# Kernel optimization log

Hardware: AMD Instinct MI355X
Metric: run time of the kernel (lower is better)

## Reference

```python
import jax, jax.numpy as jnp
import numpy as np

N_NODES = 50000
N_EDGES = 800000
IN_CH = 128
HID = 16
HEADS = 8
OUT_CH = 64


def setup_inputs() -> dict:
    key = jax.random.key(0)
    ks = jax.random.split(key, 16)
    H1 = HID * HEADS  # 128
    inp = {
        "x": jax.random.normal(ks[0], (N_NODES, IN_CH), dtype=jnp.float32),
        "edge_index": jax.random.randint(ks[1], (2, N_EDGES), 0, N_NODES, dtype=jnp.int64),
        # layer 1: GATv2Conv(IN_CH -> HID, heads=HEADS, concat=True)
        "W1l": jax.random.normal(ks[2], (IN_CH, H1), dtype=jnp.float32) * 0.05,
        "W1r": jax.random.normal(ks[3], (IN_CH, H1), dtype=jnp.float32) * 0.05,
        "att1": jax.random.normal(ks[4], (HEADS, HID), dtype=jnp.float32) * 0.05,
        "b1": jnp.zeros((H1,), dtype=jnp.float32),
        "skip1_W": jax.random.normal(ks[5], (IN_CH, H1), dtype=jnp.float32) * 0.05,
        "skip1_b": jnp.zeros((H1,), dtype=jnp.float32),
        # PyG LayerNorm (default mode='graph') affine params
        "ln_w": jnp.ones((H1,), dtype=jnp.float32),
        "ln_b": jnp.zeros((H1,), dtype=jnp.float32),
        # layer 2: GATv2Conv(H1 -> OUT_CH, heads=1, concat=False)
        "W2l": jax.random.normal(ks[6], (H1, OUT_CH), dtype=jnp.float32) * 0.05,
        "W2r": jax.random.normal(ks[7], (H1, OUT_CH), dtype=jnp.float32) * 0.05,
        "att2": jax.random.normal(ks[8], (1, OUT_CH), dtype=jnp.float32) * 0.05,
        "b2": jnp.zeros((OUT_CH,), dtype=jnp.float32),
        "skip2_W": jax.random.normal(ks[9], (H1, OUT_CH), dtype=jnp.float32) * 0.05,
        "skip2_b": jnp.zeros((OUT_CH,), dtype=jnp.float32),
    }
    return inp


def _gatv2(x, src, dst, Wl, Wr, att, b, concat):
    # GATv2Conv message passing (PyG semantics, share_weights=False).
    N = x.shape[0]
    H, C = att.shape
    xl = (x @ Wl).reshape(N, H, C)  # source transform (lin_l)
    xr = (x @ Wr).reshape(N, H, C)  # target transform (lin_r)
    e = jax.nn.leaky_relu(xl[src] + xr[dst], 0.2)  # [E,H,C]
    a = jnp.einsum('ehc,hc->eh', e, att)  # attention logits [E,H]
    # segment softmax over incoming edges of each dst node (self-loops guarantee non-empty)
    m = jax.lax.stop_gradient(jax.ops.segment_max(a, dst, num_segments=N))
    p = jnp.exp(a - m[dst])
    denom = jax.ops.segment_sum(p, dst, num_segments=N)
    alpha = p / denom[dst]  # [E,H]
    out = jax.ops.segment_sum(alpha[:, :, None] * xl[src], dst, num_segments=N)  # [N,H,C]
    out = out.reshape(N, H * C) if concat else out.mean(axis=1)
    return out + b


def reference(x, edge_index, W1l, W1r, att1, b1, skip1_W, skip1_b,
              ln_w, ln_b, W2l, W2r, att2, b2, skip2_W, skip2_b):
    N = x.shape[0]
    loop = jnp.arange(N, dtype=edge_index.dtype)
    src = jnp.concatenate([edge_index[0], loop])  # add_self_loops=True (PyG default)
    dst = jnp.concatenate([edge_index[1], loop])

    # layer 1: conv + skip
    h = _gatv2(x, src, dst, W1l, W1r, att1, b1, True) + (x @ skip1_W + skip1_b)
    # PyG LayerNorm, mode='graph': normalize over all nodes and features of the graph
    mu = h.mean()
    var = jnp.mean((h - mu) ** 2)
    h = ln_w * (h - mu) / jnp.sqrt(var + 1e-5) + ln_b
    h = jax.nn.elu(h)
    # dropout: inference mode -> identity

    # layer 2: conv (heads=1, concat=False) + skip
    out = _gatv2(h, src, dst, W2l, W2r, att2, b2, False) + (h @ skip2_W + skip2_b)
    return out
```

## Files before the change

### kernel.cpp

```cpp
#include <hip/hip_runtime.h>
#include <math.h>

#define NND 50000
#define NE0 800000
#define NET 850000
#define SCAN_B 196

using short8 = __attribute__((ext_vector_type(8))) short;
using f32x4  = __attribute__((ext_vector_type(4))) float;

__device__ __forceinline__ float lrelu(float v) { return v > 0.f ? v : 0.2f * v; }

__device__ __forceinline__ unsigned short f2bf(float f) {
    unsigned int u = __float_as_uint(f);
    u = (u + 0x7fff + ((u >> 16) & 1)) >> 16;
    return (unsigned short)u;
}
__device__ __forceinline__ float2 bf2x2(unsigned int u) {
    float2 r;
    r.x = __uint_as_float(u << 16);
    r.y = __uint_as_float(u & 0xffff0000u);
    return r;
}

template <int CTRL>
__device__ __forceinline__ float dpp_add(float v) {
    int j = __builtin_amdgcn_update_dpp(0, __float_as_int(v), CTRL, 0xf, 0xf, true);
    return v + __int_as_float(j);
}

__global__ __launch_bounds__(256) void wt_prep(const float* __restrict__ S0,
                                               const float* __restrict__ S1,
                                               const float* __restrict__ S2,
                                               unsigned short* __restrict__ T0,
                                               unsigned short* __restrict__ T1,
                                               unsigned short* __restrict__ T2, int N) {
    int per = 128 * N, total = 3 * per;
    for (int idx = blockIdx.x * blockDim.x + threadIdx.x; idx < total;
         idx += gridDim.x * blockDim.x) {
        int which = idx / per;
        int rem = idx - which * per;
        int k = rem / N, n = rem - k * N;
        const float* S = which == 0 ? S0 : (which == 1 ? S1 : S2);
        unsigned short* T = which == 0 ? T0 : (which == 1 ? T1 : T2);
        T[n * 128 + k] = f2bf(S[rem]);
    }
}

template <int BN, bool LN>
__global__ __launch_bounds__(256) void gemm3_mfma(
    const float* __restrict__ A,
    const unsigned short* __restrict__ Bt0, const unsigned short* __restrict__ Bt1,
    const unsigned short* __restrict__ Bt2, const float* __restrict__ bias2,
    unsigned short* __restrict__ C0, unsigned short* __restrict__ C1, float* __restrict__ C2,
    const float* __restrict__ musig, const float* __restrict__ lnw,
    const float* __restrict__ lnb, int M) {
    __shared__ __align__(16) unsigned short As[64 * 128];
    const int tid = threadIdx.x;
    const int m0 = blockIdx.x * 64;

    float mu = 0.f, rinv = 1.f;
    if constexpr (LN) { mu = musig[0]; rinv = musig[1]; }

    {
        const int row = tid >> 2, qc = tid & 3;
        const int gm = m0 + row;
        const float* Ar = A + (size_t)gm * 128;
#pragma unroll
        for (int i = 0; i < 4; i++) {
            int k0 = qc * 32 + i * 8;
            float v[8];
            if (gm < M) {
                float4 a0 = *(const float4*)(Ar + k0);
                float4 a1 = *(const float4*)(Ar + k0 + 4);
                v[0] = a0.x; v[1] = a0.y; v[2] = a0.z; v[3] = a0.w;
                v[4] = a1.x; v[5] = a1.y; v[6] = a1.z; v[7] = a1.w;
            } else {
#pragma unroll
                for (int j = 0; j < 8; j++) v[j] = 0.f;
            }
            if constexpr (LN) {
                float4 w0 = *(const float4*)(lnw + k0);
                float4 w1 = *(const float4*)(lnw + k0 + 4);
                float4 b0 = *(const float4*)(lnb + k0);
                float4 b1 = *(const float4*)(lnb + k0 + 4);
                float wv[8] = {w0.x, w0.y, w0.z, w0.w, w1.x, w1.y, w1.z, w1.w};
                float bv[8] = {b0.x, b0.y, b0.z, b0.w, b1.x, b1.y, b1.z, b1.w};
#pragma unroll
                for (int j = 0; j < 8; j++) {
                    float t = wv[j] * (v[j] - mu) * rinv + bv[j];
                    v[j] = t > 0.f ? t : __expf(t) - 1.f;
                }
            }
            short8 pk;
#pragma unroll
            for (int j = 0; j < 8; j++) pk[j] = (short)f2bf(v[j]);
            *(short8*)&As[row * 128 + (k0 ^ ((row & 7) << 3))] = pk;
        }
    }
    __syncthreads();

    const int lane = tid & 63;
    const int wid = tid >> 6;
    const int lr = lane & 15;
    const int lk = lane >> 4;

    short8 a[4][4];
#pragma unroll
    for (int rf = 0; rf < 4; rf++) {
        int row = rf * 16 + lr;
#pragma unroll
        for (int kc = 0; kc < 4; kc++) {
            int k0 = kc * 32 + lk * 8;
            a[rf][kc] = *(short8*)&As[row * 128 + (k0 ^ ((row & 7) << 3))];
        }
    }

    constexpr int NCF = BN / 64;
    const int nbase = wid * (BN / 4);

    const unsigned short* Bts[3] = {Bt0, Bt1, Bt2};
#pragma unroll
    for (int j = 0; j < 3; j++) {
        const unsigned short* Bt = Bts[j];
        short8 b[NCF][4];
#pragma unroll
        for (int cf = 0; cf < NCF; cf++) {
            int n = nbase + cf * 16 + lr;
#pragma unroll
            for (int kc = 0; kc < 4; kc++)
                b[cf][kc] = *(const short8*)(Bt + (size_t)n * 128 + kc * 32 + lk * 8);
        }
        f32x4 acc[4][NCF];
#pragma unroll
        for (int rf = 0; rf < 4; rf++)
#pragma unroll
            for (int cf = 0; cf < NCF; cf++) acc[rf][cf] = (f32x4){0.f, 0.f, 0.f, 0.f};
#pragma unroll
        for (int kc = 0; kc < 4; kc++)
#pragma unroll
            for (int rf = 0; rf < 4; rf++)
#pragma unroll
                for (int cf = 0; cf < NCF; cf++)
                    acc[rf][cf] = __builtin_amdgcn_mfma_f32_16x16x32_bf16(
                        a[rf][kc], b[cf][kc], acc[rf][cf], 0, 0, 0);
        if (j < 2) {
            unsigned short* C = (j == 0) ? C0 : C1;
#pragma unroll
            for (int rf = 0; rf < 4; rf++)
#pragma unroll
                for (int cf = 0; cf < NCF; cf++) {
                    int col = nbase + cf * 16 + lr;
#pragma unroll
                    for (int r = 0; r < 4; r++) {
                        int row = m0 + rf * 16 + lk * 4 + r;
                        if (row < M) C[(size_t)row * BN + col] = f2bf(acc[rf][cf][r]);
                    }
                }
        } else {
#pragma unroll
            for (int rf = 0; rf < 4; rf++)
#pragma unroll
                for (int cf = 0; cf < NCF; cf++) {
                    int col = nbase + cf * 16 + lr;
                    float bb = bias2[col];
#pragma unroll
                    for (int r = 0; r < 4; r++) {
                        int row = m0 + rf * 16 + lk * 4 + r;
                        if (row < M) C2[(size_t)row * BN + col] = acc[rf][cf][r] + bb;
                    }
                }
        }
    }
}

__global__ __launch_bounds__(256) void csr_count(const int* __restrict__ ei, int* __restrict__ deg) {
    int i = blockIdx.x * blockDim.x + threadIdx.x;
    int stride = gridDim.x * blockDim.x;
    for (int e = i; e < NE0; e += stride) atomicAdd(&deg[ei[NE0 + e]], 1);
}

__global__ __launch_bounds__(256) void scan1(const int* __restrict__ deg,
                                             int* __restrict__ locexc,
                                             int* __restrict__ blocksum) {
    __shared__ int s[256];
    const int t = threadIdx.x;
    const int g = blockIdx.x * 256 + t;
    int v = (g < NND) ? deg[g] + 1 : 0;
    s[t] = v;
    __syncthreads();
    for (int off = 1; off < 256; off <<= 1) {
        int x = (t >= off) ? s[t - off] : 0;
        __syncthreads();
        s[t] += x;
        __syncthreads();
    }
    if (g < NND) locexc[g] = s[t] - v;
    if (t == 255) blocksum[blockIdx.x] = s[255];
}

__global__ __launch_bounds__(256) void scan2(const int* __restrict__ blocksum,
                                             int* __restrict__ blockoff,
                                             int* __restrict__ rowptr) {
    __shared__ int s[256];
    const int t = threadIdx.x;
    int v = (t < SCAN_B) ? blocksum[t] : 0;
    s[t] = v;
    __syncthreads();
    for (int off = 1; off < 256; off <<= 1) {
        int x = (t >= off) ? s[t - off] : 0;
        __syncthreads();
        s[t] += x;
        __syncthreads();
    }
    if (t < SCAN_B) blockoff[t] = s[t] - v;
    if (t == 255) rowptr[NND] = s[255];
}

__global__ __launch_bounds__(256) void scan3(const int* __restrict__ locexc,
                                             const int* __restrict__ blockoff,
                                             int* __restrict__ rowptr,
                                             int* __restrict__ csrs) {
    const int g = blockIdx.x * 256 + threadIdx.x;
    if (g < NND) {
        int rp = locexc[g] + blockoff[g >> 8];
        rowptr[g] = rp;
        csrs[rp] = g;
    }
}

__global__ __launch_bounds__(256) void csr_fill(const int* __restrict__ ei,
                                                const int* __restrict__ rowptr,
                                                int* __restrict__ cursor,
                                                int* __restrict__ csrs) {
    int i = blockIdx.x * blockDim.x + threadIdx.x;
    int stride = gridDim.x * blockDim.x;
    for (int e = i; e < NE0; e += stride) {
        int s = ei[e], d = ei[NE0 + e];
        int pos = atomicAdd(&cursor[d], 1);
        csrs[rowptr[d] + 1 + pos] = s;
    }
}

__global__ __launch_bounds__(256) void aggr_l1(const int* __restrict__ rowptr,
                                               const int* __restrict__ csrs,
                                               const unsigned short* __restrict__ xl,
                                               const unsigned short* __restrict__ xr,
                                               const float* __restrict__ att,
                                               const float* __restrict__ b1,
                                               float* __restrict__ h,
                                               float2* __restrict__ partial) {
    const int lane = threadIdx.x & 63;
    const int wv = threadIdx.x >> 6;
    int wid = (blockIdx.x * blockDim.x + threadIdx.x) >> 6;
    const int nw = (gridDim.x * blockDim.x) >> 6;
    const int c = lane * 2;
    float2 attv = *(const float2*)(att + c);
    float2 b1v = *(const float2*)(b1 + c);
    float ts = 0.f, ts2 = 0.f;
    for (int d = wid; d < NND; d += nw) {
        int p0 = rowptr[d], p1 = rowptr[d + 1];
        float2 xrv = bf2x2(*(const unsigned int*)(xr + (size_t)d * 128 + c));
        float den0 = 0.f, den1 = 0.f, den2 = 0.f, den3 = 0.f;
        float a00 = 0.f, a01 = 0.f, a10 = 0.f, a11 = 0.f;
        float a20 = 0.f, a21 = 0.f, a30 = 0.f, a31 = 0.f;
        int i = p0;
        for (; i + 4 <= p1; i += 4) {
            int s0 = csrs[i], s1 = csrs[i + 1], s2 = csrs[i + 2], s3 = csrs[i + 3];
            float2 x0 = bf2x2(*(const unsigned int*)(xl + (size_t)s0 * 128 + c));
            float2 x1 = bf2x2(*(const unsigned int*)(xl + (size_t)s1 * 128 + c));
            float2 x2 = bf2x2(*(const unsigned int*)(xl + (size_t)s2 * 128 + c));
            float2 x3 = bf2x2(*(const unsigned int*)(xl + (size_t)s3 * 128 + c));
            float q0 = lrelu(x0.x + xrv.x) * attv.x + lrelu(x0.y + xrv.y) * attv.y;
            float q1 = lrelu(x1.x + xrv.x) * attv.x + lrelu(x1.y + xrv.y) * attv.y;
            float q2 = lrelu(x2.x + xrv.x) * attv.x + lrelu(x2.y + xrv.y) * attv.y;
            float q3 = lrelu(x3.x + xrv.x) * attv.x + lrelu(x3.y + xrv.y) * attv.y;
            q0 = dpp_add<0xB1>(q0); q0 = dpp_add<0x4E>(q0); q0 = dpp_add<0x141>(q0);
            q1 = dpp_add<0xB1>(q1); q1 = dpp_add<0x4E>(q1); q1 = dpp_add<0x141>(q1);
            q2 = dpp_add<0xB1>(q2); q2 = dpp_add<0x4E>(q2); q2 = dpp_add<0x141>(q2);
            q3 = dpp_add<0xB1>(q3); q3 = dpp_add<0x4E>(q3); q3 = dpp_add<0x141>(q3);
            float p0v = __expf(q0), p1v = __expf(q1), p2v = __expf(q2), p3v = __expf(q3);
            den0 += p0v; a00 = fmaf(p0v, x0.x, a00); a01 = fmaf(p0v, x0.y, a01);
            den1 += p1v; a10 = fmaf(p1v, x1.x, a10); a11 = fmaf(p1v, x1.y, a11);
            den2 += p2v; a20 = fmaf(p2v, x2.x, a20); a21 = fmaf(p2v, x2.y, a21);
            den3 += p3v; a30 = fmaf(p3v, x3.x, a30); a31 = fmaf(p3v, x3.y, a31);
        }
        for (; i < p1; i++) {
            int s0 = csrs[i];
            float2 x0 = bf2x2(*(const unsigned int*)(xl + (size_t)s0 * 128 + c));
            float q0 = lrelu(x0.x + xrv.x) * attv.x + lrelu(x0.y + xrv.y) * attv.y;
            q0 = dpp_add<0xB1>(q0); q0 = dpp_add<0x4E>(q0); q0 = dpp_add<0x141>(q0);
            float p0v = __expf(q0);
            den0 += p0v; a00 = fmaf(p0v, x0.x, a00); a01 = fmaf(p0v, x0.y, a01);
        }
        float den = (den0 + den1) + (den2 + den3);
        float a0 = (a00 + a10) + (a20 + a30);
        float a1 = (a01 + a11) + (a21 + a31);
        float inv = 1.f / den;
        float2 hv = *(float2*)(h + (size_t)d * 128 + c);
        hv.x += a0 * inv + b1v.x;
        hv.y += a1 * inv + b1v.y;
        *(float2*)(h + (size_t)d * 128 + c) = hv;
        ts += hv.x + hv.y;
        ts2 += hv.x * hv.x + hv.y * hv.y;
    }
    __shared__ float red[8];
#pragma unroll
    for (int off = 32; off; off >>= 1) {
        ts += __shfl_down(ts, off);
        ts2 += __shfl_down(ts2, off);
    }
    if (lane == 0) { red[wv * 2] = ts; red[wv * 2 + 1] = ts2; }
    __syncthreads();
    if (threadIdx.x == 0) {
        float s = red[0] + red[2] + red[4] + red[6];
        float s2 = red[1] + red[3] + red[5] + red[7];
        partial[blockIdx.x] = make_float2(s, s2);
    }
}

__global__ __launch_bounds__(256) void ln_final2(const float2* __restrict__ part, int np,
                                                 float* __restrict__ musig) {
    double s = 0.0, s2 = 0.0;
    for (int i = threadIdx.x; i < np; i += 256) {
        float2 p = part[i];
        s += p.x;
        s2 += p.y;
    }
#pragma unroll
    for (int off = 32; off; off >>= 1) {
        s += __shfl_down(s, off);
        s2 += __shfl_down(s2, off);
    }
    __shared__ double red[8];
    const int wv = threadIdx.x >> 6;
    if ((threadIdx.x & 63) == 0) { red[wv * 2] = s; red[wv * 2 + 1] = s2; }
    __syncthreads();
    if (threadIdx.x == 0) {
        double S = red[0] + red[2] + red[4] + red[6];
        double S2 = red[1] + red[3] + red[5] + red[7];
        double inv_n = 1.0 / ((double)NND * 128.0);
        double mu = S * inv_n;
        double var = S2 * inv_n - mu * mu;
        musig[0] = (float)mu;
        musig[1] = (float)(1.0 / sqrt(var + 1e-5));
    }
}

__global__ __launch_bounds__(256) void aggr_l2(const int* __restrict__ rowptr,
                                               const int* __restrict__ csrs,
                                               const unsigned short* __restrict__ xl,
                                               const unsigned short* __restrict__ xr,
                                               const float* __restrict__ att,
                                               const float* __restrict__ b2,
                                               float* __restrict__ out) {
    const int hl = threadIdx.x & 31;
    int hwid = (blockIdx.x * blockDim.x + threadIdx.x) >> 5;
    const int nhw = (gridDim.x * blockDim.x) >> 5;
    const int c = hl * 2;
    float2 attv = *(const float2*)(att + c);
    float2 b2v = *(const float2*)(b2 + c);
    for (int d = hwid; d < NND; d += nhw) {
        int p0 = rowptr[d], p1 = rowptr[d + 1];
        float2 xrv = bf2x2(*(const unsigned int*)(xr + (size_t)d * 64 + c));
        float den0 = 0.f, den1 = 0.f, den2 = 0.f, den3 = 0.f;
        float a00 = 0.f, a01 = 0.f, a10 = 0.f, a11 = 0.f;
        float a20 = 0.f, a21 = 0.f, a30 = 0.f, a31 = 0.f;
        int i = p0;
        for (; i + 4 <= p1; i += 4) {
            int s0 = csrs[i], s1 = csrs[i + 1], s2 = csrs[i + 2], s3 = csrs[i + 3];
            float2 x0 = bf2x2(*(const unsigned int*)(xl + (size_t)s0 * 64 + c));
            float2 x1 = bf2x2(*(const unsigned int*)(xl + (size_t)s1 * 64 + c));
            float2 x2 = bf2x2(*(const unsigned int*)(xl + (size_t)s2 * 64 + c));
            float2 x3 = bf2x2(*(const unsigned int*)(xl + (size_t)s3 * 64 + c));
            float q0 = lrelu(x0.x + xrv.x) * attv.x + lrelu(x0.y + xrv.y) * attv.y;
            float q1 = lrelu(x1.x + xrv.x) * attv.x + lrelu(x1.y + xrv.y) * attv.y;
            float q2 = lrelu(x2.x + xrv.x) * attv.x + lrelu(x2.y + xrv.y) * attv.y;
            float q3 = lrelu(x3.x + xrv.x) * attv.x + lrelu(x3.y + xrv.y) * attv.y;
            q0 = dpp_add<0xB1>(q0); q0 = dpp_add<0x4E>(q0); q0 = dpp_add<0x141>(q0);
            q0 = dpp_add<0x140>(q0); q0 += __shfl_xor(q0, 16);
            q1 = dpp_add<0xB1>(q1); q1 = dpp_add<0x4E>(q1); q1 = dpp_add<0x141>(q1);
            q1 = dpp_add<0x140>(q1); q1 += __shfl_xor(q1, 16);
            q2 = dpp_add<0xB1>(q2); q2 = dpp_add<0x4E>(q2); q2 = dpp_add<0x141>(q2);
            q2 = dpp_add<0x140>(q2); q2 += __shfl_xor(q2, 16);
            q3 = dpp_add<0xB1>(q3); q3 = dpp_add<0x4E>(q3); q3 = dpp_add<0x141>(q3);
            q3 = dpp_add<0x140>(q3); q3 += __shfl_xor(q3, 16);
            float p0v = __expf(q0), p1v = __expf(q1), p2v = __expf(q2), p3v = __expf(q3);
            den0 += p0v; a00 = fmaf(p0v, x0.x, a00); a01 = fmaf(p0v, x0.y, a01);
            den1 += p1v; a10 = fmaf(p1v, x1.x, a10); a11 = fmaf(p1v, x1.y, a11);
            den2 += p2v; a20 = fmaf(p2v, x2.x, a20); a21 = fmaf(p2v, x2.y, a21);
            den3 += p3v; a30 = fmaf(p3v, x3.x, a30); a31 = fmaf(p3v, x3.y, a31);
        }
        for (; i < p1; i++) {
            int s0 = csrs[i];
            float2 x0 = bf2x2(*(const unsigned int*)(xl + (size_t)s0 * 64 + c));
            float q0 = lrelu(x0.x + xrv.x) * attv.x + lrelu(x0.y + xrv.y) * attv.y;
            q0 = dpp_add<0xB1>(q0); q0 = dpp_add<0x4E>(q0); q0 = dpp_add<0x141>(q0);
            q0 = dpp_add<0x140>(q0); q0 += __shfl_xor(q0, 16);
            float p0v = __expf(q0);
            den0 += p0v; a00 = fmaf(p0v, x0.x, a00); a01 = fmaf(p0v, x0.y, a01);
        }
        float den = (den0 + den1) + (den2 + den3);
        float a0 = (a00 + a10) + (a20 + a30);
        float a1 = (a01 + a11) + (a21 + a31);
        float inv = 1.f / den;
        float2 ov = *(float2*)(out + (size_t)d * 64 + c);
        ov.x += a0 * inv + b2v.x;
        ov.y += a1 * inv + b2v.y;
        *(float2*)(out + (size_t)d * 64 + c) = ov;
    }
}

extern "C" void kernel_launch(void* const* d_in, const int* in_sizes, int n_in,
                              void* d_out, int out_size, void* d_ws, size_t ws_size,
                              hipStream_t stream) {
    (void)in_sizes; (void)n_in; (void)out_size; (void)ws_size;
    const float* x    = (const float*)d_in[0];
    const int*   ei   = (const int*)d_in[1];
    const float* W1l  = (const float*)d_in[2];
    const float* W1r  = (const float*)d_in[3];
    const float* att1 = (const float*)d_in[4];
    const float* b1   = (const float*)d_in[5];
    const float* s1W  = (const float*)d_in[6];
    const float* s1b  = (const float*)d_in[7];
    const float* lnw  = (const float*)d_in[8];
    const float* lnb  = (const float*)d_in[9];
    const float* W2l  = (const float*)d_in[10];
    const float* W2r  = (const float*)d_in[11];
    const float* att2 = (const float*)d_in[12];
    const float* b2   = (const float*)d_in[13];
    const float* s2W  = (const float*)d_in[14];
    const float* s2b  = (const float*)d_in[15];
    float* out = (float*)d_out;

    char* ws = (char*)d_ws;
    size_t off = 0;
    auto alloc = [&](size_t bytes) {
        size_t o = off;
        off = (off + bytes + 255) & ~(size_t)255;
        return o;
    };
    unsigned short* xl = (unsigned short*)(ws + alloc((size_t)NND * 128 * 2));
    unsigned short* xr = (unsigned short*)(ws + alloc((size_t)NND * 128 * 2));
    float* h     = (float*)(ws + alloc((size_t)NND * 128 * 4));
    int* deg     = (int*)(ws + alloc((size_t)NND * 4));
    int* rowptr  = (int*)(ws + alloc((size_t)(NND + 1) * 4));
    int* cursor  = (int*)(ws + alloc((size_t)NND * 4));
    int* csrs    = (int*)(ws + alloc((size_t)NET * 4));
    int* locexc  = (int*)(ws + alloc((size_t)NND * 4));
    int* blocksum= (int*)(ws + alloc((size_t)SCAN_B * 4));
    int* blockoff= (int*)(ws + alloc((size_t)SCAN_B * 4));
    unsigned short* Bt1 = (unsigned short*)(ws + alloc((size_t)3 * 128 * 128 * 2));
    unsigned short* Bt2 = (unsigned short*)(ws + alloc((size_t)3 * 64 * 128 * 2));
    float2* partial = (float2*)(ws + alloc((size_t)12500 * 8));
    float* musig = (float*)(ws + alloc(8));

    hipMemsetAsync(deg, 0, (size_t)NND * 4, stream);
    hipMemsetAsync(cursor, 0, (size_t)NND * 4, stream);

    csr_count<<<1024, 256, 0, stream>>>(ei, deg);
    scan1<<<SCAN_B, 256, 0, stream>>>(deg, locexc, blocksum);
    scan2<<<1, 256, 0, stream>>>(blocksum, blockoff, rowptr);
    scan3<<<SCAN_B, 256, 0, stream>>>(locexc, blockoff, rowptr, csrs);
    csr_fill<<<1024, 256, 0, stream>>>(ei, rowptr, cursor, csrs);

    wt_prep<<<192, 256, 0, stream>>>(W1l, W1r, s1W, Bt1, Bt1 + 16384, Bt1 + 32768, 128);
    wt_prep<<<96, 256, 0, stream>>>(W2l, W2r, s2W, Bt2, Bt2 + 8192, Bt2 + 16384, 64);

    gemm3_mfma<128, false><<<782, 256, 0, stream>>>(x, Bt1, Bt1 + 16384, Bt1 + 32768, s1b,
                                                    xl, xr, h, nullptr, nullptr, nullptr, NND);
    aggr_l1<<<12500, 256, 0, stream>>>(rowptr, csrs, xl, xr, att1, b1, h, partial);
    ln_final2<<<1, 256, 0, stream>>>(partial, 12500, musig);

    gemm3_mfma<64, true><<<782, 256, 0, stream>>>(h, Bt2, Bt2 + 8192, Bt2 + 16384, s2b,
                                                  xl, xr, out, musig, lnw, lnb, NND);
    aggr_l2<<<6250, 256, 0, stream>>>(rowptr, csrs, xl, xr, att2, b2, out);
}
```

Baseline: 251.8 us.

## Store layer-1 hidden state in bf16, unroll aggregation by 8, merge weight prep

The intermediate h buffer (skip output plus layer-1 aggregation) now lives in bf16 instead of fp32, which halves its write and read traffic across the GEMM, aggregation and second GEMM. The layer-1 aggregation loop is unrolled to eight neighbours per iteration with clamped indices and masked logits, so the scalar tail loop is gone and more gathers are in flight. The two weight-prep launches are merged into one kernel, and leaky ReLU becomes an fmax. The price is extra rounding in h before LayerNorm statistics and layer 2, plus wasted gathers on padded lanes for low-degree nodes.

```diff
diff --git a/kernel.cpp b/kernel.cpp
--- a/kernel.cpp
+++ b/kernel.cpp
@@ -6,10 +6,11 @@
 #define NET 850000
 #define SCAN_B 196
 
-using short8 = __attribute__((ext_vector_type(8))) short;
-using f32x4  = __attribute__((ext_vector_type(4))) float;
-
-__device__ __forceinline__ float lrelu(float v) { return v > 0.f ? v : 0.2f * v; }
+using short8  = __attribute__((ext_vector_type(8))) short;
+using ushort8 = __attribute__((ext_vector_type(8))) unsigned short;
+using f32x4   = __attribute__((ext_vector_type(4))) float;
+
+__device__ __forceinline__ float lrelu(float v) { return fmaxf(v, 0.2f * v); }
 
 __device__ __forceinline__ unsigned short f2bf(float f) {
     unsigned int u = __float_as_uint(f);
@@ -22,6 +23,9 @@
     r.y = __uint_as_float(u & 0xffff0000u);
     return r;
 }
+__device__ __forceinline__ unsigned int packbf(float x, float y) {
+    return (unsigned int)f2bf(x) | ((unsigned int)f2bf(y) << 16);
+}
 
 template <int CTRL>
 __device__ __forceinline__ float dpp_add(float v) {
@@ -29,30 +33,34 @@
     return v + __int_as_float(j);
 }
 
-__global__ __launch_bounds__(256) void wt_prep(const float* __restrict__ S0,
-                                               const float* __restrict__ S1,
-                                               const float* __restrict__ S2,
-                                               unsigned short* __restrict__ T0,
-                                               unsigned short* __restrict__ T1,
-                                               unsigned short* __restrict__ T2, int N) {
-    int per = 128 * N, total = 3 * per;
-    for (int idx = blockIdx.x * blockDim.x + threadIdx.x; idx < total;
-         idx += gridDim.x * blockDim.x) {
-        int which = idx / per;
-        int rem = idx - which * per;
-        int k = rem / N, n = rem - k * N;
-        const float* S = which == 0 ? S0 : (which == 1 ? S1 : S2);
-        unsigned short* T = which == 0 ? T0 : (which == 1 ? T1 : T2);
-        T[n * 128 + k] = f2bf(S[rem]);
-    }
-}
-
-template <int BN, bool LN>
+__global__ __launch_bounds__(256) void wt_prep_all(
+    const float* __restrict__ A0, const float* __restrict__ A1, const float* __restrict__ A2,
+    const float* __restrict__ B0, const float* __restrict__ B1, const float* __restrict__ B2,
+    unsigned short* __restrict__ T1, unsigned short* __restrict__ T2) {
+    const int L1 = 3 * 128 * 128;
+    const int L2 = 3 * 64 * 128;
+    int idx = blockIdx.x * blockDim.x + threadIdx.x;
+    if (idx < L1) {
+        int which = idx / 16384, rem = idx - which * 16384;
+        int k = rem >> 7, n = rem & 127;
+        const float* S = which == 0 ? A0 : (which == 1 ? A1 : A2);
+        T1[which * 16384 + n * 128 + k] = f2bf(S[rem]);
+    } else if (idx < L1 + L2) {
+        int idx2 = idx - L1;
+        int which = idx2 / 8192, rem = idx2 - which * 8192;
+        int k = rem >> 6, n = rem & 63;
+        const float* S = which == 0 ? B0 : (which == 1 ? B1 : B2);
+        T2[which * 8192 + n * 128 + k] = f2bf(S[rem]);
+    }
+}
+
+template <int BN, bool LN, bool OUTBF>
 __global__ __launch_bounds__(256) void gemm3_mfma(
-    const float* __restrict__ A,
+    const void* __restrict__ Av,
     const unsigned short* __restrict__ Bt0, const unsigned short* __restrict__ Bt1,
     const unsigned short* __restrict__ Bt2, const float* __restrict__ bias2,
-    unsigned short* __restrict__ C0, unsigned short* __restrict__ C1, float* __restrict__ C2,
+    unsigned short* __restrict__ C0, unsigned short* __restrict__ C1,
+    unsigned short* __restrict__ C2b, float* __restrict__ C2f,
     const float* __restrict__ musig, const float* __restrict__ lnw,
     const float* __restrict__ lnb, int M) {
     __shared__ __align__(16) unsigned short As[64 * 128];
@@ -65,21 +73,20 @@
     {
         const int row = tid >> 2, qc = tid & 3;
         const int gm = m0 + row;
-        const float* Ar = A + (size_t)gm * 128;
 #pragma unroll
         for (int i = 0; i < 4; i++) {
             int k0 = qc * 32 + i * 8;
             float v[8];
-            if (gm < M) {
-                float4 a0 = *(const float4*)(Ar + k0);
-                float4 a1 = *(const float4*)(Ar + k0 + 4);
-                v[0] = a0.x; v[1] = a0.y; v[2] = a0.z; v[3] = a0.w;
-                v[4] = a1.x; v[5] = a1.y; v[6] = a1.z; v[7] = a1.w;
-            } else {
-#pragma unroll
-                for (int j = 0; j < 8; j++) v[j] = 0.f;
-            }
             if constexpr (LN) {
+                const unsigned short* A = (const unsigned short*)Av;
+                if (gm < M) {
+                    ushort8 us = *(const ushort8*)(A + (size_t)gm * 128 + k0);
+#pragma unroll
+                    for (int j = 0; j < 8; j++) v[j] = __uint_as_float((unsigned int)us[j] << 16);
+                } else {
+#pragma unroll
+                    for (int j = 0; j < 8; j++) v[j] = 0.f;
+                }
                 float4 w0 = *(const float4*)(lnw + k0);
                 float4 w1 = *(const float4*)(lnw + k0 + 4);
                 float4 b0 = *(const float4*)(lnb + k0);
@@ -91,6 +98,17 @@
                     float t = wv[j] * (v[j] - mu) * rinv + bv[j];
                     v[j] = t > 0.f ? t : __expf(t) - 1.f;
                 }
+            } else {
+                const float* A = (const float*)Av;
+                if (gm < M) {
+                    float4 a0 = *(const float4*)(A + (size_t)gm * 128 + k0);
+                    float4 a1 = *(const float4*)(A + (size_t)gm * 128 + k0 + 4);
+                    v[0] = a0.x; v[1] = a0.y; v[2] = a0.z; v[3] = a0.w;
+                    v[4] = a1.x; v[5] = a1.y; v[6] = a1.z; v[7] = a1.w;
+                } else {
+#pragma unroll
+                    for (int j = 0; j < 8; j++) v[j] = 0.f;
+                }
             }
             short8 pk;
 #pragma unroll
@@ -167,7 +185,12 @@
 #pragma unroll
                     for (int r = 0; r < 4; r++) {
                         int row = m0 + rf * 16 + lk * 4 + r;
-                        if (row < M) C2[(size_t)row * BN + col] = acc[rf][cf][r] + bb;
+                        if (row < M) {
+                            if constexpr (OUTBF)
+                                C2b[(size_t)row * BN + col] = f2bf(acc[rf][cf][r] + bb);
+                            else
+                                C2f[(size_t)row * BN + col] = acc[rf][cf][r] + bb;
+                        }
                     }
                 }
         }
@@ -248,7 +271,7 @@
                                                const unsigned short* __restrict__ xr,
                                                const float* __restrict__ att,
                                                const float* __restrict__ b1,
-                                               float* __restrict__ h,
+                                               unsigned short* __restrict__ h,
                                                float2* __restrict__ partial) {
     const int lane = threadIdx.x & 63;
     const int wv = threadIdx.x >> 6;
@@ -260,47 +283,65 @@
     float ts = 0.f, ts2 = 0.f;
     for (int d = wid; d < NND; d += nw) {
         int p0 = rowptr[d], p1 = rowptr[d + 1];
+        const int p1m1 = p1 - 1;
         float2 xrv = bf2x2(*(const unsigned int*)(xr + (size_t)d * 128 + c));
         float den0 = 0.f, den1 = 0.f, den2 = 0.f, den3 = 0.f;
         float a00 = 0.f, a01 = 0.f, a10 = 0.f, a11 = 0.f;
         float a20 = 0.f, a21 = 0.f, a30 = 0.f, a31 = 0.f;
-        int i = p0;
-        for (; i + 4 <= p1; i += 4) {
-            int s0 = csrs[i], s1 = csrs[i + 1], s2 = csrs[i + 2], s3 = csrs[i + 3];
-            float2 x0 = bf2x2(*(const unsigned int*)(xl + (size_t)s0 * 128 + c));
-            float2 x1 = bf2x2(*(const unsigned int*)(xl + (size_t)s1 * 128 + c));
-            float2 x2 = bf2x2(*(const unsigned int*)(xl + (size_t)s2 * 128 + c));
-            float2 x3 = bf2x2(*(const unsigned int*)(xl + (size_t)s3 * 128 + c));
+        for (int i = p0; i < p1; i += 8) {
+            int idx[8];
+#pragma unroll
+            for (int j = 0; j < 8; j++) idx[j] = csrs[min(i + j, p1m1)];
+            unsigned int u[8];
+#pragma unroll
+            for (int j = 0; j < 8; j++)
+                u[j] = *(const unsigned int*)(xl + (size_t)idx[j] * 128 + c);
+            float2 x0 = bf2x2(u[0]), x1 = bf2x2(u[1]), x2 = bf2x2(u[2]), x3 = bf2x2(u[3]);
+            float2 x4 = bf2x2(u[4]), x5 = bf2x2(u[5]), x6 = bf2x2(u[6]), x7 = bf2x2(u[7]);
             float q0 = lrelu(x0.x + xrv.x) * attv.x + lrelu(x0.y + xrv.y) * attv.y;
             float q1 = lrelu(x1.x + xrv.x) * attv.x + lrelu(x1.y + xrv.y) * attv.y;
             float q2 = lrelu(x2.x + xrv.x) * attv.x + lrelu(x2.y + xrv.y) * attv.y;
             float q3 = lrelu(x3.x + xrv.x) * attv.x + lrelu(x3.y + xrv.y) * attv.y;
+            float q4 = lrelu(x4.x + xrv.x) * attv.x + lrelu(x4.y + xrv.y) * attv.y;
+            float q5 = lrelu(x5.x + xrv.x) * attv.x + lrelu(x5.y + xrv.y) * attv.y;
+            float q6 = lrelu(x6.x + xrv.x) * attv.x + lrelu(x6.y + xrv.y) * attv.y;
+            float q7 = lrelu(x7.x + xrv.x) * attv.x + lrelu(x7.y + xrv.y) * attv.y;
             q0 = dpp_add<0xB1>(q0); q0 = dpp_add<0x4E>(q0); q0 = dpp_add<0x141>(q0);
             q1 = dpp_add<0xB1>(q1); q1 = dpp_add<0x4E>(q1); q1 = dpp_add<0x141>(q1);
             q2 = dpp_add<0xB1>(q2); q2 = dpp_add<0x4E>(q2); q2 = dpp_add<0x141>(q2);
             q3 = dpp_add<0xB1>(q3); q3 = dpp_add<0x4E>(q3); q3 = dpp_add<0x141>(q3);
+            q4 = dpp_add<0xB1>(q4); q4 = dpp_add<0x4E>(q4); q4 = dpp_add<0x141>(q4);
+            q5 = dpp_add<0xB1>(q5); q5 = dpp_add<0x4E>(q5); q5 = dpp_add<0x141>(q5);
+            q6 = dpp_add<0xB1>(q6); q6 = dpp_add<0x4E>(q6); q6 = dpp_add<0x141>(q6);
+            q7 = dpp_add<0xB1>(q7); q7 = dpp_add<0x4E>(q7); q7 = dpp_add<0x141>(q7);
+            q0 = (i + 0 < p1) ? q0 : -30.f;
+            q1 = (i + 1 < p1) ? q1 : -30.f;
+            q2 = (i + 2 < p1) ? q2 : -30.f;
+            q3 = (i + 3 < p1) ? q3 : -30.f;
+            q4 = (i + 4 < p1) ? q4 : -30.f;
+            q5 = (i + 5 < p1) ? q5 : -30.f;
+            q6 = (i + 6 < p1) ? q6 : -30.f;
+            q7 = (i + 7 < p1) ? q7 : -30.f;
             float p0v = __expf(q0), p1v = __expf(q1), p2v = __expf(q2), p3v = __expf(q3);
+            float p4v = __expf(q4), p5v = __expf(q5), p6v = __expf(q6), p7v = __expf(q7);
             den0 += p0v; a00 = fmaf(p0v, x0.x, a00); a01 = fmaf(p0v, x0.y, a01);
             den1 += p1v; a10 = fmaf(p1v, x1.x, a10); a11 = fmaf(p1v, x1.y, a11);
             den2 += p2v; a20 = fmaf(p2v, x2.x, a20); a21 = fmaf(p2v, x2.y, a21);
             den3 += p3v; a30 = fmaf(p3v, x3.x, a30); a31 = fmaf(p3v, x3.y, a31);
-        }
-        for (; i < p1; i++) {
-            int s0 = csrs[i];
-            float2 x0 = bf2x2(*(const unsigned int*)(xl + (size_t)s0 * 128 + c));
-            float q0 = lrelu(x0.x + xrv.x) * attv.x + lrelu(x0.y + xrv.y) * attv.y;
-            q0 = dpp_add<0xB1>(q0); q0 = dpp_add<0x4E>(q0); q0 = dpp_add<0x141>(q0);
-            float p0v = __expf(q0);
-            den0 += p0v; a00 = fmaf(p0v, x0.x, a00); a01 = fmaf(p0v, x0.y, a01);
+            den0 += p4v; a00 = fmaf(p4v, x4.x, a00); a01 = fmaf(p4v, x4.y, a01);
+            den1 += p5v; a10 = fmaf(p5v, x5.x, a10); a11 = fmaf(p5v, x5.y, a11);
+            den2 += p6v; a20 = fmaf(p6v, x6.x, a20); a21 = fmaf(p6v, x6.y, a21);
+            den3 += p7v; a30 = fmaf(p7v, x7.x, a30); a31 = fmaf(p7v, x7.y, a31);
         }
         float den = (den0 + den1) + (den2 + den3);
         float a0 = (a00 + a10) + (a20 + a30);
         float a1 = (a01 + a11) + (a21 + a31);
         float inv = 1.f / den;
-        float2 hv = *(float2*)(h + (size_t)d * 128 + c);
+        unsigned int* hp = (unsigned int*)(h + (size_t)d * 128 + c);
+        float2 hv = bf2x2(*hp);
         hv.x += a0 * inv + b1v.x;
         hv.y += a1 * inv + b1v.y;
-        *(float2*)(h + (size_t)d * 128 + c) = hv;
+        *hp = packbf(hv.x, hv.y);
         ts += hv.x + hv.y;
         ts2 += hv.x * hv.x + hv.y * hv.y;
     }
@@ -442,7 +483,7 @@
     };
     unsigned short* xl = (unsigned short*)(ws + alloc((size_t)NND * 128 * 2));
     unsigned short* xr = (unsigned short*)(ws + alloc((size_t)NND * 128 * 2));
-    float* h     = (float*)(ws + alloc((size_t)NND * 128 * 4));
+    unsigned short* h  = (unsigned short*)(ws + alloc((size_t)NND * 128 * 2));
     int* deg     = (int*)(ws + alloc((size_t)NND * 4));
     int* rowptr  = (int*)(ws + alloc((size_t)(NND + 1) * 4));
     int* cursor  = (int*)(ws + alloc((size_t)NND * 4));
@@ -464,15 +505,16 @@
     scan3<<<SCAN_B, 256, 0, stream>>>(locexc, blockoff, rowptr, csrs);
     csr_fill<<<1024, 256, 0, stream>>>(ei, rowptr, cursor, csrs);
 
-    wt_prep<<<192, 256, 0, stream>>>(W1l, W1r, s1W, Bt1, Bt1 + 16384, Bt1 + 32768, 128);
-    wt_prep<<<96, 256, 0, stream>>>(W2l, W2r, s2W, Bt2, Bt2 + 8192, Bt2 + 16384, 64);
-
-    gemm3_mfma<128, false><<<782, 256, 0, stream>>>(x, Bt1, Bt1 + 16384, Bt1 + 32768, s1b,
-                                                    xl, xr, h, nullptr, nullptr, nullptr, NND);
+    wt_prep_all<<<288, 256, 0, stream>>>(W1l, W1r, s1W, W2l, W2r, s2W, Bt1, Bt2);
+
+    gemm3_mfma<128, false, true><<<782, 256, 0, stream>>>(
+        (const void*)x, Bt1, Bt1 + 16384, Bt1 + 32768, s1b,
+        xl, xr, h, nullptr, nullptr, nullptr, nullptr, NND);
     aggr_l1<<<12500, 256, 0, stream>>>(rowptr, csrs, xl, xr, att1, b1, h, partial);
     ln_final2<<<1, 256, 0, stream>>>(partial, 12500, musig);
 
-    gemm3_mfma<64, true><<<782, 256, 0, stream>>>(h, Bt2, Bt2 + 8192, Bt2 + 16384, s2b,
-                                                  xl, xr, out, musig, lnw, lnb, NND);
+    gemm3_mfma<64, true, false><<<782, 256, 0, stream>>>(
+        (const void*)h, Bt2, Bt2 + 8192, Bt2 + 16384, s2b,
+        xl, xr, nullptr, out, musig, lnw, lnb, NND);
     aggr_l2<<<6250, 256, 0, stream>>>(rowptr, csrs, xl, xr, att2, b2, out);
 }
```

Measured after the change: 270.0 us. +7.2%, slower.
